# Kernel tuning notes

Measured on AMD Instinct MI355X. Metric: run time of the kernel, lower is better.

## Reference

```python
import jax, jax.numpy as jnp
import numpy as np

N = 50000      # nodes (single node type 'tx')
E = 400000     # edges per edge type ('fwd' and 'rev')
F_IN = 128     # input feature dim
F = 128        # cfg.gnn.dim_inner
H = 8          # attention heads
D = F // H     # per-head dim
L = 2          # cfg.gnn.layers_mp
C = 2          # dim_out (fraud logits)


def setup_inputs() -> dict:
    key = jax.random.key(0)
    k = jax.random.split(key, 12)
    f32 = jnp.float32
    g = lambda kk, sh, fan: jax.random.normal(kk, sh, f32) / np.float32(np.sqrt(fan))
    return dict(
        x=jax.random.normal(k[0], (N, F_IN), f32),
        edge_index_fwd=jax.random.randint(k[1], (2, E), 0, N),
        edge_index_rev=jax.random.randint(k[2], (2, E), 0, N),
        in_w=g(k[3], (F_IN, F), F_IN),
        in_b=jnp.zeros((F,), f32),
        kqv_w=g(k[4], (L, F, 3 * F), F),
        kqv_b=jnp.zeros((L, 3 * F), f32),
        krel_w=g(k[5], (L, 2, H, D, D), D),
        vrel_w=g(k[6], (L, 2, H, D, D), D),
        p_rel=jnp.ones((L, 2, H), f32),
        out_w=g(k[7], (L, F, F), F),
        out_b=jnp.zeros((L, F), f32),
        skip=jnp.ones((L,), f32),
        head_w=g(k[8], (F, C), F),
        head_b=jnp.zeros((C,), f32),
    )


def reference(x, edge_index_fwd, edge_index_rev, in_w, in_b, kqv_w, kqv_b,
              krel_w, vrel_w, p_rel, out_w, out_b, skip, head_w, head_b):
    n = x.shape[0]
    ef, er = edge_index_fwd, edge_index_rev
    Ef, Er = ef.shape[1], er.shape[1]
    dst = jnp.concatenate([ef[1], er[1]])                 # [E_tot]
    scale = 1.0 / jnp.sqrt(jnp.asarray(D, x.dtype))

    h = x @ in_w + in_b                                   # in_proj['tx'], [N,F]
    for l in range(L):
        kqv = h @ kqv_w[l] + kqv_b[l]                     # [N,3F]
        k, q, v = jnp.split(kqv, 3, axis=1)
        k = k.reshape(n, H, D)
        q = q.reshape(n, H, D)
        v = v.reshape(n, H, D)
        # per-edge-type relation transforms (head-wise DxD, no bias)
        k_rel = jnp.einsum('nhd,ehdf->enhf', k, krel_w[l])  # [2,N,H,D]
        v_rel = jnp.einsum('nhd,ehdf->enhf', v, vrel_w[l])
        # gather src features per edge type, concatenate edge types
        k_j = jnp.concatenate([k_rel[0][ef[0]], k_rel[1][er[0]]], axis=0)  # [E_tot,H,D]
        v_j = jnp.concatenate([v_rel[0][ef[0]], v_rel[1][er[0]]], axis=0)
        p_e = jnp.concatenate([jnp.broadcast_to(p_rel[l, 0], (Ef, H)),
                               jnp.broadcast_to(p_rel[l, 1], (Er, H))], axis=0)
        q_i = q[dst]                                       # [E_tot,H,D]
        alpha = jnp.einsum('ehd,ehd->eh', q_i, k_j) * p_e * scale
        # segment softmax over all incoming edges of each dst node
        m = jax.ops.segment_max(alpha, dst, num_segments=n)
        ex = jnp.exp(alpha - m[dst])
        denom = jax.ops.segment_sum(ex, dst, num_segments=n)
        w = ex / (denom[dst] + 1e-16)                      # [E_tot,H]
        agg = jax.ops.segment_sum(w[:, :, None] * v_j, dst,
                                  num_segments=n).reshape(n, F)
        a = jax.nn.gelu(agg, approximate=False) @ out_w[l] + out_b[l]
        g = jax.nn.sigmoid(skip[l])
        h = jax.nn.relu(g * a + (1.0 - g) * h)             # skip + act(dropout=0)
    return h @ head_w + head_b                             # logits [N,C]
```

## Files before the change

### kernel.cpp

```cpp
#include <hip/hip_runtime.h>
#include <math.h>

typedef short short8 __attribute__((ext_vector_type(8)));
typedef float f32x4 __attribute__((ext_vector_type(4)));

#define CAP 64

__device__ __forceinline__ unsigned short f2bf(float f){
    unsigned u = __float_as_uint(f);
    unsigned r = u + 0x7fffu + ((u >> 16) & 1u);
    return (unsigned short)(r >> 16);
}
__device__ __forceinline__ float bf2f(unsigned short s){
    return __uint_as_float((unsigned)s << 16);
}

__global__ void k_setup(const float* __restrict__ kqv_w, const float* __restrict__ kqv_b,
                        const float* __restrict__ krel_w, const float* __restrict__ vrel_w,
                        const float* __restrict__ p_rel, const float* __restrict__ out_w,
                        const float* __restrict__ out_b, const float* __restrict__ in_w,
                        const float* __restrict__ x, const float* __restrict__ head_b,
                        const int* __restrict__ ef, const int* __restrict__ er,
                        unsigned short* __restrict__ WcT, float* __restrict__ biasc,
                        unsigned short* __restrict__ WoT, float* __restrict__ biaso,
                        unsigned short* __restrict__ WiT, unsigned short* __restrict__ x16,
                        int* __restrict__ cnt, unsigned* __restrict__ srcs_pad,
                        float* __restrict__ logits, int n_nodes, int Ef, int Er)
{
    const long long E0 = Ef + Er;
    const long long N0 = E0 + 2*129*640;
    const long long N1 = N0 + 2*129*128;
    const long long N2 = N1 + 128*128;
    const long long N3 = N2 + (long long)n_nodes*32;
    const long long N4 = N3 + 2*n_nodes;

    for (long long idx = (long long)blockIdx.x*blockDim.x + threadIdx.x; idx < N4;
         idx += (long long)gridDim.x*blockDim.x) {
        if (idx < E0) {
            int e = (int)idx;
            int src, dst, tt;
            if (e < Ef) { src = ef[e]; dst = ef[Ef + e]; tt = 0; }
            else { int e2 = e - Ef; src = er[e2]; dst = er[Er + e2]; tt = 1; }
            int pos = atomicAdd(&cnt[dst], 1);
            if (pos < CAP)
                srcs_pad[dst*CAP + pos] = (unsigned)(tt*n_nodes + src)*32u;
        } else if (idx < N0) {
            int i = (int)(idx - E0);
            int l = i / (129*640);
            int rem = i % (129*640);
            int r = rem / 640, c = rem % 640;
            float val;
            if (c < 128) {
                val = (r < 128) ? kqv_w[((size_t)l*128 + r)*384 + 128 + c]
                                : kqv_b[l*384 + 128 + c];
            } else {
                int c2 = c - 128;
                int tt = c2 >> 8;
                int cc = c2 & 255;
                int f = cc >> 1;
                int part = cc & 1;
                int hh = f >> 4, fd = f & 15;
                const float* rw = (part == 0 ? krel_w : vrel_w)
                                  + (((size_t)(l*2 + tt)*8 + hh)*16)*16 + fd;
                int base_col = (part == 0 ? 0 : 256) + hh*16;
                float s = 0.f;
                #pragma unroll
                for (int d = 0; d < 16; ++d) {
                    float a = (r < 128) ? kqv_w[((size_t)l*128 + r)*384 + base_col + d]
                                        : kqv_b[l*384 + base_col + d];
                    s += a * rw[d*16];
                }
                if (part == 0) s *= p_rel[(l*2 + tt)*8 + hh] * 0.25f * 1.4426950408889634f;
                val = s;
            }
            if (r < 128) WcT[((size_t)l*640 + c)*128 + r] = f2bf(val);
            else         biasc[l*640 + c] = val;
        } else if (idx < N1) {
            int i = (int)(idx - N0);
            int l = i / (129*128);
            int rem = i % (129*128);
            int r = rem / 128, c = rem % 128;
            if (r < 128) WoT[((size_t)l*128 + c)*128 + r] = f2bf(out_w[((size_t)l*128 + r)*128 + c]);
            else         biaso[l*128 + c] = out_b[l*128 + c];
        } else if (idx < N2) {
            int i = (int)(idx - N1);
            int r = i >> 7, c = i & 127;
            WiT[(size_t)c*128 + r] = f2bf(in_w[(size_t)r*128 + c]);
        } else if (idx < N3) {
            long long i = idx - N2;
            float4 v = *(const float4*)&x[i*4];
            uint2 w;
            w.x = (unsigned)f2bf(v.x) | ((unsigned)f2bf(v.y) << 16);
            w.y = (unsigned)f2bf(v.z) | ((unsigned)f2bf(v.w) << 16);
            *(uint2*)&x16[i*4] = w;
        } else {
            long long i = idx - N3;
            logits[i] = head_b[i & 1];
        }
    }
}

__global__ __launch_bounds__(256) void k_mfma(
    const unsigned short* __restrict__ A16, const unsigned short* __restrict__ WT,
    const float* __restrict__ biasc, unsigned short* __restrict__ q16,
    unsigned short* __restrict__ h16, unsigned* __restrict__ kv,
    const float* __restrict__ skip, const float* __restrict__ hw,
    float* __restrict__ logits, int l,
    int n_nodes, int R, int C, int mode)
{
    __shared__ uint4 As[64*16];
    __shared__ uint4 Ws[64*16];
    int b = blockIdx.x;
    int xcd = b & 7, jj = b >> 3;
    int r_t = (jj / C)*8 + xcd;
    int c_t = jj % C;
    if (r_t >= R) return;
    int n0 = r_t*64, c0 = c_t*64;
    int t = threadIdx.x;

    #pragma unroll
    for (int it = 0; it < 4; ++it) {
        int gi = t + it*256;
        int m = gi >> 4, g = gi & 15;
        uint4 a = *(const uint4*)&A16[((size_t)(n0 + m)*16 + g)*8];
        As[m*16 + (g ^ (m & 15))] = a;
    }
    #pragma unroll
    for (int it = 0; it < 4; ++it) {
        int gi = t + it*256;
        int cw = gi >> 4, g = gi & 15;
        uint4 wv = *(const uint4*)&WT[((size_t)(c0 + cw)*16 + g)*8];
        Ws[cw*16 + (g ^ (cw & 15))] = wv;
    }
    __syncthreads();

    int lane = t & 63, w = t >> 6;
    int lm = lane & 15, quad = lane >> 4;
    f32x4 acc[4];
    #pragma unroll
    for (int i = 0; i < 4; ++i) { acc[i][0]=0.f; acc[i][1]=0.f; acc[i][2]=0.f; acc[i][3]=0.f; }

    #pragma unroll
    for (int chunk = 0; chunk < 4; ++chunk) {
        int gq = chunk*4 + quad;
        short8 bfrag = *(const short8*)&Ws[(w*16 + lm)*16 + (gq ^ lm)];
        #pragma unroll
        for (int i = 0; i < 4; ++i) {
            short8 afrag = *(const short8*)&As[(i*16 + lm)*16 + (gq ^ lm)];
            acc[i] = __builtin_amdgcn_mfma_f32_16x16x32_bf16(afrag, bfrag, acc[i], 0, 0, 0);
        }
    }

    int c = c0 + w*16 + lm;
    float bc = biasc[c];
    bool even = (lane & 1) == 0;
    if (mode == 3) {
        float g = 1.f/(1.f + expf(-skip[l]));
        float hw0 = hw[c*2], hw1 = hw[c*2 + 1];
        #pragma unroll
        for (int i = 0; i < 4; ++i) {
            #pragma unroll
            for (int rr = 0; rr < 4; ++rr) {
                int m = n0 + i*16 + quad*4 + rr;
                float nv = 0.f;
                if (m < n_nodes) {
                    float hv = bf2f(h16[(size_t)m*128 + c]);
                    nv = fmaxf(g*(acc[i][rr] + bc) + (1.f - g)*hv, 0.f);
                }
                float p0 = nv*hw0, p1 = nv*hw1;
                p0 += __shfl_xor(p0, 1); p1 += __shfl_xor(p1, 1);
                p0 += __shfl_xor(p0, 2); p1 += __shfl_xor(p1, 2);
                p0 += __shfl_xor(p0, 4); p1 += __shfl_xor(p1, 4);
                p0 += __shfl_xor(p0, 8); p1 += __shfl_xor(p1, 8);
                if (lm == 0 && m < n_nodes) {
                    atomicAdd(&logits[m*2],     p0);
                    atomicAdd(&logits[m*2 + 1], p1);
                }
            }
        }
    } else if (mode == 2) {
        float g = 1.f/(1.f + expf(-skip[l]));
        unsigned* dst = (unsigned*)h16;
        #pragma unroll
        for (int i = 0; i < 4; ++i) {
            #pragma unroll
            for (int rr = 0; rr < 4; ++rr) {
                int m = n0 + i*16 + quad*4 + rr;
                float hv = (m < n_nodes) ? bf2f(h16[(size_t)m*128 + c]) : 0.f;
                float nv = fmaxf(g*(acc[i][rr] + bc) + (1.f - g)*hv, 0.f);
                float other = __shfl_xor(nv, 1);
                if (even && m < n_nodes)
                    dst[(size_t)m*64 + (c >> 1)] =
                        (unsigned)f2bf(nv) | ((unsigned)f2bf(other) << 16);
            }
        }
    } else if (mode == 0) {
        unsigned* dst = (unsigned*)h16;
        #pragma unroll
        for (int i = 0; i < 4; ++i) {
            #pragma unroll
            for (int rr = 0; rr < 4; ++rr) {
                int m = n0 + i*16 + quad*4 + rr;
                float nv = acc[i][rr] + bc;
                float other = __shfl_xor(nv, 1);
                if (even && m < n_nodes)
                    dst[(size_t)m*64 + (c >> 1)] =
                        (unsigned)f2bf(nv) | ((unsigned)f2bf(other) << 16);
            }
        }
    } else if (c0 < 128) {
        unsigned* dst = (unsigned*)q16;
        #pragma unroll
        for (int i = 0; i < 4; ++i) {
            #pragma unroll
            for (int rr = 0; rr < 4; ++rr) {
                float val = acc[i][rr] + bc;
                float other = __shfl_xor(val, 1);
                int m = n0 + i*16 + quad*4 + rr;
                if (even && m < n_nodes)
                    dst[(size_t)m*64 + (c >> 1)] =
                        (unsigned)f2bf(val) | ((unsigned)f2bf(other) << 16);
            }
        }
    } else {
        int c2 = c - 128;
        int tt = c2 >> 8;
        int f = (c2 & 255) >> 1;
        unsigned* dst = kv + (size_t)tt*n_nodes*128;
        #pragma unroll
        for (int i = 0; i < 4; ++i) {
            #pragma unroll
            for (int rr = 0; rr < 4; ++rr) {
                float val = acc[i][rr] + bc;
                float other = __shfl_xor(val, 1);
                int m = n0 + i*16 + quad*4 + rr;
                if (even && m < n_nodes) {
                    unsigned wd = ((unsigned)f2bf(val) << 16) | (unsigned)f2bf(other);
                    dst[(size_t)m*128 + f] = wd;
                }
            }
        }
    }
}

__global__ __launch_bounds__(256) void k_attn(
    const unsigned* __restrict__ srcs_pad, const int* __restrict__ cnt,
    const uint4* __restrict__ kv, const unsigned short* __restrict__ q16,
    unsigned short* __restrict__ qa16, int n_base, int n_hi)
{
    int lane = threadIdx.x & 31;
    int n = n_base + blockIdx.x*8 + (threadIdx.x >> 5);
    if (n >= n_hi) return;
    uint2 qp = *(const uint2*)&q16[(size_t)n*128 + lane*4];
    float4 q4;
    q4.x = __uint_as_float(qp.x << 16);
    q4.y = __uint_as_float(qp.x & 0xffff0000u);
    q4.z = __uint_as_float(qp.y << 16);
    q4.w = __uint_as_float(qp.y & 0xffff0000u);
    int s = n*CAP, e = s + min(cnt[n], CAP);

    const uint4* kvl = kv + lane;
    const unsigned* srcs = srcs_pad;

    float lsum = 0.f;
    float4 a = make_float4(0.f, 0.f, 0.f, 0.f);

    unsigned sv0 = srcs[s],     sv1 = srcs[s + 1];
    unsigned sv2 = srcs[s + 2], sv3 = srcs[s + 3];
    uint4 w0 = kvl[sv0], w1 = kvl[sv1], w2 = kvl[sv2], w3 = kvl[sv3];

    int pos = s;

#define ATT_PAIR(wA, wB)                                                       \
    {                                                                          \
        float d0 = __uint_as_float(wA.x & 0xffff0000u)*q4.x                    \
                 + __uint_as_float(wA.y & 0xffff0000u)*q4.y                    \
                 + __uint_as_float(wA.z & 0xffff0000u)*q4.z                    \
                 + __uint_as_float(wA.w & 0xffff0000u)*q4.w;                   \
        float d1 = __uint_as_float(wB.x & 0xffff0000u)*q4.x                    \
                 + __uint_as_float(wB.y & 0xffff0000u)*q4.y                    \
                 + __uint_as_float(wB.z & 0xffff0000u)*q4.z                    \
                 + __uint_as_float(wB.w & 0xffff0000u)*q4.w;                   \
        d0 += __shfl_xor(d0, 1); d1 += __shfl_xor(d1, 1);                      \
        d0 += __shfl_xor(d0, 2); d1 += __shfl_xor(d1, 2);                      \
        float wt0 = exp2f(d0), wt1 = exp2f(d1);                                \
        lsum += wt0 + wt1;                                                     \
        a.x += wt0*__uint_as_float(wA.x << 16);                                \
        a.y += wt0*__uint_as_float(wA.y << 16);                                \
        a.z += wt0*__uint_as_float(wA.z << 16);                                \
        a.w += wt0*__uint_as_float(wA.w << 16);                                \
        a.x += wt1*__uint_as_float(wB.x << 16);                                \
        a.y += wt1*__uint_as_float(wB.y << 16);                                \
        a.z += wt1*__uint_as_float(wB.z << 16);                                \
        a.w += wt1*__uint_as_float(wB.w << 16);                                \
    }

#define ATT_ONE(wA)                                                            \
    {                                                                          \
        float d = __uint_as_float(wA.x & 0xffff0000u)*q4.x                     \
                + __uint_as_float(wA.y & 0xffff0000u)*q4.y                     \
                + __uint_as_float(wA.z & 0xffff0000u)*q4.z                     \
                + __uint_as_float(wA.w & 0xffff0000u)*q4.w;                    \
        d += __shfl_xor(d, 1);                                                 \
        d += __shfl_xor(d, 2);                                                 \
        float wt = exp2f(d);                                                   \
        lsum += wt;                                                            \
        a.x += wt*__uint_as_float(wA.x << 16);                                 \
        a.y += wt*__uint_as_float(wA.y << 16);                                 \
        a.z += wt*__uint_as_float(wA.z << 16);                                 \
        a.w += wt*__uint_as_float(wA.w << 16);                                 \
    }

    for (; pos + 3 < e; pos += 4) {
        unsigned p0 = srcs[pos + 4], p1 = srcs[pos + 5];
        ATT_PAIR(w0, w1);
        w0 = kvl[p0]; w1 = kvl[p1];
        unsigned p2 = srcs[pos + 6], p3 = srcs[pos + 7];
        ATT_PAIR(w2, w3);
        w2 = kvl[p2]; w3 = kvl[p3];
    }
    int rem = e - pos;
    if (rem > 0) {
        ATT_ONE(w0);
        if (rem > 1) ATT_ONE(w1);
        if (rem > 2) ATT_ONE(w2);
    }
#undef ATT_PAIR
#undef ATT_ONE

    float inv = 1.f/(lsum + 1e-16f);
    float x0 = a.x*inv, x1 = a.y*inv, x2 = a.z*inv, x3 = a.w*inv;
    float g0 = 0.5f*x0*(1.f + erff(x0*0.70710678118654752f));
    float g1 = 0.5f*x1*(1.f + erff(x1*0.70710678118654752f));
    float g2 = 0.5f*x2*(1.f + erff(x2*0.70710678118654752f));
    float g3 = 0.5f*x3*(1.f + erff(x3*0.70710678118654752f));
    uint2 pk;
    pk.x = (unsigned)f2bf(g0) | ((unsigned)f2bf(g1) << 16);
    pk.y = (unsigned)f2bf(g2) | ((unsigned)f2bf(g3) << 16);
    *(uint2*)&qa16[(size_t)n*128 + lane*4] = pk;
}

extern "C" void kernel_launch(void* const* d_in, const int* in_sizes, int n_in,
                              void* d_out, int out_size, void* d_ws, size_t ws_size,
                              hipStream_t stream)
{
    const float* x      = (const float*)d_in[0];
    const int*   ef     = (const int*)d_in[1];
    const int*   er     = (const int*)d_in[2];
    const float* in_w   = (const float*)d_in[3];
    const float* in_b   = (const float*)d_in[4];
    const float* kqv_w  = (const float*)d_in[5];
    const float* kqv_b  = (const float*)d_in[6];
    const float* krel_w = (const float*)d_in[7];
    const float* vrel_w = (const float*)d_in[8];
    const float* p_rel  = (const float*)d_in[9];
    const float* out_w  = (const float*)d_in[10];
    const float* out_b  = (const float*)d_in[11];
    const float* skip   = (const float*)d_in[12];
    const float* head_w = (const float*)d_in[13];
    const float* head_b = (const float*)d_in[14];
    float* out = (float*)d_out;

    int n_nodes = in_sizes[0] / 128;
    int Ef = in_sizes[1] / 2, Er = in_sizes[2] / 2;
    int ntile = (n_nodes + 63)/64;
    int npad = ntile*64;

    float* p = (float*)d_ws;
    unsigned* kv = (unsigned*)p; p += (size_t)2*n_nodes*128;
    unsigned short* h16  = (unsigned short*)p; p += (size_t)npad*128/2;
    unsigned short* q16  = (unsigned short*)p; p += (size_t)npad*128/2;
    unsigned short* qa16 = (unsigned short*)p; p += (size_t)npad*128/2;
    unsigned short* x16  = (unsigned short*)p; p += (size_t)npad*128/2;
    unsigned short* WiT = (unsigned short*)p; p += (size_t)(128*128)/2;
    unsigned short* WcT = (unsigned short*)p; p += (size_t)(2*640*128)/2;
    float* biasc = p; p += 2*640;
    unsigned short* WoT = (unsigned short*)p; p += (size_t)(2*128*128)/2;
    float* biaso = p; p += 2*128;
    int* cnt = (int*)p;            p += n_nodes;
    unsigned* srcs_pad = (unsigned*)p; p += (size_t)n_nodes*CAP;

    int Rg = (ntile + 7)/8;

    hipMemsetAsync(cnt, 0, (size_t)n_nodes*sizeof(int), stream);
    hipMemsetAsync(srcs_pad, 0, (size_t)n_nodes*CAP*sizeof(unsigned), stream);
    k_setup<<<7500, 256, 0, stream>>>(kqv_w, kqv_b, krel_w, vrel_w, p_rel, out_w, out_b,
                                      in_w, x, head_b, ef, er, WcT, biasc, WoT, biaso,
                                      WiT, x16, cnt, srcs_pad, out, n_nodes, Ef, Er);

    int nh = (((n_nodes + 1)/2) + 7) & ~7;
    if (nh > n_nodes) nh = n_nodes;

    k_mfma<<<Rg*8*2, 256, 0, stream>>>(x16, WiT, in_b, nullptr, h16, kv, skip,
                                       head_w, out, 0, n_nodes, ntile, 2, 0);
    for (int l = 0; l < 2; ++l) {
        k_mfma<<<Rg*8*10, 256, 0, stream>>>(h16, WcT + (size_t)l*640*128,
                                            biasc + l*640, q16, nullptr, kv, skip,
                                            head_w, out, l, n_nodes, ntile, 10, 1);
        k_attn<<<nh/8, 256, 0, stream>>>(srcs_pad, cnt, (const uint4*)kv, q16, qa16,
                                         0, nh);
        k_attn<<<(n_nodes - nh + 7)/8, 256, 0, stream>>>(srcs_pad, cnt, (const uint4*)kv,
                                                         q16, qa16, nh, n_nodes);
        int omode = (l == 1) ? 3 : 2;
        k_mfma<<<Rg*8*2, 256, 0, stream>>>(qa16, WoT + (size_t)l*128*128,
                                           biaso + l*128, nullptr, h16, kv, skip,
                                           head_w, out, l, n_nodes, ntile, 2, omode);
    }
}
```

Baseline: 394.6 us.

## Build padded adjacency via two-pass per-XCD binning with LDS scatter

Replaces the per-edge global atomic scatter into the padded source list with two passes. First, edges are appended to per-XCD, per-64-node-bin buffers. Then a new kernel gathers each bin, scatters entries into LDS slots using shared atomics, and writes srcs_pad and cnt coalesced. This also removes the large memset of srcs_pad and the cnt memset. The cost is an extra kernel launch and intermediate buffer traffic, and edges beyond a bin capacity of 512 per XCD are silently dropped.

Result: slower. 405.2 us (+2.7%).

```diff
diff --git a/kernel.cpp b/kernel.cpp
--- a/kernel.cpp
+++ b/kernel.cpp
@@ -5,6 +5,7 @@
 typedef float f32x4 __attribute__((ext_vector_type(4)));
 
 #define CAP 64
+#define BCAP 512
 
 __device__ __forceinline__ unsigned short f2bf(float f){
     unsigned u = __float_as_uint(f);
@@ -24,9 +25,13 @@
                         unsigned short* __restrict__ WcT, float* __restrict__ biasc,
                         unsigned short* __restrict__ WoT, float* __restrict__ biaso,
                         unsigned short* __restrict__ WiT, unsigned short* __restrict__ x16,
-                        int* __restrict__ cnt, unsigned* __restrict__ srcs_pad,
-                        float* __restrict__ logits, int n_nodes, int Ef, int Er)
+                        int* __restrict__ bcur, unsigned* __restrict__ bbuf,
+                        float* __restrict__ logits, int n_nodes, int Ef, int Er, int NB)
 {
+    int xcd;
+    asm volatile("s_getreg_b32 %0, hwreg(HW_REG_XCC_ID)" : "=s"(xcd));
+    xcd &= 7;
+
     const long long E0 = Ef + Er;
     const long long N0 = E0 + 2*129*640;
     const long long N1 = N0 + 2*129*128;
@@ -41,9 +46,12 @@
             int src, dst, tt;
             if (e < Ef) { src = ef[e]; dst = ef[Ef + e]; tt = 0; }
             else { int e2 = e - Ef; src = er[e2]; dst = er[Er + e2]; tt = 1; }
-            int pos = atomicAdd(&cnt[dst], 1);
-            if (pos < CAP)
-                srcs_pad[dst*CAP + pos] = (unsigned)(tt*n_nodes + src)*32u;
+            int r = dst >> 6;
+            int seg = xcd*NB + r;
+            int pos = atomicAdd(&bcur[seg], 1);
+            if (pos < BCAP)
+                bbuf[(size_t)seg*BCAP + pos] =
+                    (unsigned)(dst & 63) | ((unsigned)tt << 6) | ((unsigned)src << 7);
         } else if (idx < N0) {
             int i = (int)(idx - E0);
             int l = i / (129*640);
@@ -100,6 +108,44 @@
     }
 }
 
+__global__ __launch_bounds__(256) void k_bin2(
+    const unsigned* __restrict__ bbuf, const int* __restrict__ bcur,
+    unsigned* __restrict__ srcs_pad, int* __restrict__ cnt,
+    int n_nodes, int NB)
+{
+    __shared__ unsigned lslot[64*CAP];
+    __shared__ int lcnt[64];
+    int r = blockIdx.x;
+    int lo = r*64;
+    int m = min(64, n_nodes - lo);
+    if (m <= 0) return;
+    int t = threadIdx.x;
+    if (t < 64) lcnt[t] = 0;
+    __syncthreads();
+    for (int xc = 0; xc < 8; ++xc) {
+        int seg = xc*NB + r;
+        int n = min(bcur[seg], BCAP);
+        const unsigned* sp = &bbuf[(size_t)seg*BCAP];
+        for (int i = t; i < n; i += 256) {
+            unsigned w = sp[i];
+            int d = w & 63;
+            int p = atomicAdd(&lcnt[d], 1);
+            if (p < CAP) {
+                unsigned tt = (w >> 6) & 1u;
+                unsigned src = w >> 7;
+                lslot[d*CAP + p] = (tt*(unsigned)n_nodes + src)*32u;
+            }
+        }
+    }
+    __syncthreads();
+    for (int i = t; i < m*CAP; i += 256) {
+        int d = i >> 6, s = i & (CAP - 1);
+        int c = min(lcnt[d], CAP);
+        srcs_pad[(size_t)(lo + d)*CAP + s] = (s < c) ? lslot[d*CAP + s] : 0u;
+    }
+    if (t < m) cnt[lo + t] = min(lcnt[t], CAP);
+}
+
 __global__ __launch_bounds__(256) void k_mfma(
     const unsigned short* __restrict__ A16, const unsigned short* __restrict__ WT,
     const float* __restrict__ biasc, unsigned short* __restrict__ q16,
@@ -365,6 +411,7 @@
     int Ef = in_sizes[1] / 2, Er = in_sizes[2] / 2;
     int ntile = (n_nodes + 63)/64;
     int npad = ntile*64;
+    int NB = (n_nodes + 63)/64;
 
     float* p = (float*)d_ws;
     unsigned* kv = (unsigned*)p; p += (size_t)2*n_nodes*128;
@@ -378,15 +425,17 @@
     unsigned short* WoT = (unsigned short*)p; p += (size_t)(2*128*128)/2;
     float* biaso = p; p += 2*128;
     int* cnt = (int*)p;            p += n_nodes;
+    int* bcur = (int*)p;           p += (size_t)8*NB;
+    unsigned* bbuf = (unsigned*)p; p += (size_t)8*NB*BCAP;
     unsigned* srcs_pad = (unsigned*)p; p += (size_t)n_nodes*CAP;
 
     int Rg = (ntile + 7)/8;
 
-    hipMemsetAsync(cnt, 0, (size_t)n_nodes*sizeof(int), stream);
-    hipMemsetAsync(srcs_pad, 0, (size_t)n_nodes*CAP*sizeof(unsigned), stream);
+    hipMemsetAsync(bcur, 0, (size_t)8*NB*sizeof(int), stream);
     k_setup<<<7500, 256, 0, stream>>>(kqv_w, kqv_b, krel_w, vrel_w, p_rel, out_w, out_b,
                                       in_w, x, head_b, ef, er, WcT, biasc, WoT, biaso,
-                                      WiT, x16, cnt, srcs_pad, out, n_nodes, Ef, Er);
+                                      WiT, x16, bcur, bbuf, out, n_nodes, Ef, Er, NB);
+    k_bin2<<<NB, 256, 0, stream>>>(bbuf, bcur, srcs_pad, cnt, n_nodes, NB);
 
     int nh = (((n_nodes + 1)/2) + 7) & ~7;
     if (nh > n_nodes) nh = n_nodes;
```

## Fuse input projection GEMM into setup kernel, converting x and in_w on the fly

Applied to the files above, without the earlier changes.

The separate input-projection MFMA launch and the x/in_w bf16 conversion passes are removed. The setup work and the input GEMM now run in one kernel: the first NITB blocks do edge bucketing, weight preprocessing and logits init, and the remaining blocks load fp32 x and in_w directly, convert them to bf16 into shared memory and run the MFMA. This saves one launch and the round trip of writing and rereading the x16 copy. The GEMM blocks now read fp32 inputs and do strided in_w loads, and the two kinds of blocks share one grid.

Result: slower. 416.2 us (+5.5%).

```diff
diff --git a/kernel.cpp b/kernel.cpp
--- a/kernel.cpp
+++ b/kernel.cpp
@@ -5,6 +5,7 @@
 typedef float f32x4 __attribute__((ext_vector_type(4)));
 
 #define CAP 64
+#define NITB 2048
 
 __device__ __forceinline__ unsigned short f2bf(float f){
     unsigned u = __float_as_uint(f);
@@ -15,87 +16,153 @@
     return __uint_as_float((unsigned)s << 16);
 }
 
-__global__ void k_setup(const float* __restrict__ kqv_w, const float* __restrict__ kqv_b,
-                        const float* __restrict__ krel_w, const float* __restrict__ vrel_w,
-                        const float* __restrict__ p_rel, const float* __restrict__ out_w,
-                        const float* __restrict__ out_b, const float* __restrict__ in_w,
-                        const float* __restrict__ x, const float* __restrict__ head_b,
-                        const int* __restrict__ ef, const int* __restrict__ er,
-                        unsigned short* __restrict__ WcT, float* __restrict__ biasc,
-                        unsigned short* __restrict__ WoT, float* __restrict__ biaso,
-                        unsigned short* __restrict__ WiT, unsigned short* __restrict__ x16,
-                        int* __restrict__ cnt, unsigned* __restrict__ srcs_pad,
-                        float* __restrict__ logits, int n_nodes, int Ef, int Er)
+__global__ __launch_bounds__(256) void k_front(
+        const float* __restrict__ kqv_w, const float* __restrict__ kqv_b,
+        const float* __restrict__ krel_w, const float* __restrict__ vrel_w,
+        const float* __restrict__ p_rel, const float* __restrict__ out_w,
+        const float* __restrict__ out_b, const float* __restrict__ in_w,
+        const float* __restrict__ in_b, const float* __restrict__ x,
+        const float* __restrict__ head_b,
+        const int* __restrict__ ef, const int* __restrict__ er,
+        unsigned short* __restrict__ WcT, float* __restrict__ biasc,
+        unsigned short* __restrict__ WoT, float* __restrict__ biaso,
+        int* __restrict__ cnt, unsigned* __restrict__ srcs_pad,
+        unsigned short* __restrict__ h16, float* __restrict__ logits,
+        int n_nodes, int Ef, int Er, int R)
 {
-    const long long E0 = Ef + Er;
-    const long long N0 = E0 + 2*129*640;
-    const long long N1 = N0 + 2*129*128;
-    const long long N2 = N1 + 128*128;
-    const long long N3 = N2 + (long long)n_nodes*32;
-    const long long N4 = N3 + 2*n_nodes;
-
-    for (long long idx = (long long)blockIdx.x*blockDim.x + threadIdx.x; idx < N4;
-         idx += (long long)gridDim.x*blockDim.x) {
-        if (idx < E0) {
-            int e = (int)idx;
-            int src, dst, tt;
-            if (e < Ef) { src = ef[e]; dst = ef[Ef + e]; tt = 0; }
-            else { int e2 = e - Ef; src = er[e2]; dst = er[Er + e2]; tt = 1; }
-            int pos = atomicAdd(&cnt[dst], 1);
-            if (pos < CAP)
-                srcs_pad[dst*CAP + pos] = (unsigned)(tt*n_nodes + src)*32u;
-        } else if (idx < N0) {
-            int i = (int)(idx - E0);
-            int l = i / (129*640);
-            int rem = i % (129*640);
-            int r = rem / 640, c = rem % 640;
-            float val;
-            if (c < 128) {
-                val = (r < 128) ? kqv_w[((size_t)l*128 + r)*384 + 128 + c]
-                                : kqv_b[l*384 + 128 + c];
+    if (blockIdx.x < NITB) {
+        const long long E0 = Ef + Er;
+        const long long M0 = E0 + 2*129*640;
+        const long long M1 = M0 + 2*129*128;
+        const long long M2 = M1 + 2*n_nodes;
+
+        for (long long idx = (long long)blockIdx.x*256 + threadIdx.x; idx < M2;
+             idx += (long long)NITB*256) {
+            if (idx < E0) {
+                int e = (int)idx;
+                int src, dst, tt;
+                if (e < Ef) { src = ef[e]; dst = ef[Ef + e]; tt = 0; }
+                else { int e2 = e - Ef; src = er[e2]; dst = er[Er + e2]; tt = 1; }
+                int pos = atomicAdd(&cnt[dst], 1);
+                if (pos < CAP)
+                    srcs_pad[dst*CAP + pos] = (unsigned)(tt*n_nodes + src)*32u;
+            } else if (idx < M0) {
+                int i = (int)(idx - E0);
+                int l = i / (129*640);
+                int rem = i % (129*640);
+                int r = rem / 640, c = rem % 640;
+                float val;
+                if (c < 128) {
+                    val = (r < 128) ? kqv_w[((size_t)l*128 + r)*384 + 128 + c]
+                                    : kqv_b[l*384 + 128 + c];
+                } else {
+                    int c2 = c - 128;
+                    int tt = c2 >> 8;
+                    int cc = c2 & 255;
+                    int f = cc >> 1;
+                    int part = cc & 1;
+                    int hh = f >> 4, fd = f & 15;
+                    const float* rw = (part == 0 ? krel_w : vrel_w)
+                                      + (((size_t)(l*2 + tt)*8 + hh)*16)*16 + fd;
+                    int base_col = (part == 0 ? 0 : 256) + hh*16;
+                    float s = 0.f;
+                    #pragma unroll
+                    for (int d = 0; d < 16; ++d) {
+                        float a = (r < 128) ? kqv_w[((size_t)l*128 + r)*384 + base_col + d]
+                                            : kqv_b[l*384 + base_col + d];
+                        s += a * rw[d*16];
+                    }
+                    if (part == 0) s *= p_rel[(l*2 + tt)*8 + hh] * 0.25f * 1.4426950408889634f;
+                    val = s;
+                }
+                if (r < 128) WcT[((size_t)l*640 + c)*128 + r] = f2bf(val);
+                else         biasc[l*640 + c] = val;
+            } else if (idx < M1) {
+                int i = (int)(idx - M0);
+                int l = i / (129*128);
+                int rem = i % (129*128);
+                int r = rem / 128, c = rem % 128;
+                if (r < 128) WoT[((size_t)l*128 + c)*128 + r] = f2bf(out_w[((size_t)l*128 + r)*128 + c]);
+                else         biaso[l*128 + c] = out_b[l*128 + c];
             } else {
-                int c2 = c - 128;
-                int tt = c2 >> 8;
-                int cc = c2 & 255;
-                int f = cc >> 1;
-                int part = cc & 1;
-                int hh = f >> 4, fd = f & 15;
-                const float* rw = (part == 0 ? krel_w : vrel_w)
-                                  + (((size_t)(l*2 + tt)*8 + hh)*16)*16 + fd;
-                int base_col = (part == 0 ? 0 : 256) + hh*16;
-                float s = 0.f;
-                #pragma unroll
-                for (int d = 0; d < 16; ++d) {
-                    float a = (r < 128) ? kqv_w[((size_t)l*128 + r)*384 + base_col + d]
-                                        : kqv_b[l*384 + base_col + d];
-                    s += a * rw[d*16];
-                }
-                if (part == 0) s *= p_rel[(l*2 + tt)*8 + hh] * 0.25f * 1.4426950408889634f;
-                val = s;
+                long long i = idx - M1;
+                logits[i] = head_b[i & 1];
             }
-            if (r < 128) WcT[((size_t)l*640 + c)*128 + r] = f2bf(val);
-            else         biasc[l*640 + c] = val;
-        } else if (idx < N1) {
-            int i = (int)(idx - N0);
-            int l = i / (129*128);
-            int rem = i % (129*128);
-            int r = rem / 128, c = rem % 128;
-            if (r < 128) WoT[((size_t)l*128 + c)*128 + r] = f2bf(out_w[((size_t)l*128 + r)*128 + c]);
-            else         biaso[l*128 + c] = out_b[l*128 + c];
-        } else if (idx < N2) {
-            int i = (int)(idx - N1);
-            int r = i >> 7, c = i & 127;
-            WiT[(size_t)c*128 + r] = f2bf(in_w[(size_t)r*128 + c]);
-        } else if (idx < N3) {
-            long long i = idx - N2;
-            float4 v = *(const float4*)&x[i*4];
-            uint2 w;
-            w.x = (unsigned)f2bf(v.x) | ((unsigned)f2bf(v.y) << 16);
-            w.y = (unsigned)f2bf(v.z) | ((unsigned)f2bf(v.w) << 16);
-            *(uint2*)&x16[i*4] = w;
-        } else {
-            long long i = idx - N3;
-            logits[i] = head_b[i & 1];
+        }
+        return;
+    }
+
+    __shared__ uint4 As[64*16];
+    __shared__ uint4 Ws[64*16];
+    int b = blockIdx.x - NITB;
+    int xcd = b & 7, jj = b >> 3;
+    int r_t = (jj / 2)*8 + xcd;
+    int c_t = jj % 2;
+    if (r_t >= R) return;
+    int n0 = r_t*64, c0 = c_t*64;
+    int t = threadIdx.x;
+
+    #pragma unroll
+    for (int it = 0; it < 4; ++it) {
+        int gi = t + it*256;
+        int m = gi >> 4, g = gi & 15;
+        int row = min(n0 + m, n_nodes - 1);
+        const float* xp = &x[(size_t)row*128 + g*8];
+        float4 v0 = *(const float4*)xp;
+        float4 v1 = *(const float4*)(xp + 4);
+        uint4 a;
+        a.x = (unsigned)f2bf(v0.x) | ((unsigned)f2bf(v0.y) << 16);
+        a.y = (unsigned)f2bf(v0.z) | ((unsigned)f2bf(v0.w) << 16);
+        a.z = (unsigned)f2bf(v1.x) | ((unsigned)f2bf(v1.y) << 16);
+        a.w = (unsigned)f2bf(v1.z) | ((unsigned)f2bf(v1.w) << 16);
+        As[m*16 + (g ^ (m & 15))] = a;
+    }
+    #pragma unroll
+    for (int it = 0; it < 4; ++it) {
+        int gi = t + it*256;
+        int cw = gi >> 4, g = gi & 15;
+        int col = c0 + cw;
+        const float* wp = &in_w[(size_t)(g*8)*128 + col];
+        uint4 wv;
+        wv.x = (unsigned)f2bf(wp[0])     | ((unsigned)f2bf(wp[128])   << 16);
+        wv.y = (unsigned)f2bf(wp[2*128]) | ((unsigned)f2bf(wp[3*128]) << 16);
+        wv.z = (unsigned)f2bf(wp[4*128]) | ((unsigned)f2bf(wp[5*128]) << 16);
+        wv.w = (unsigned)f2bf(wp[6*128]) | ((unsigned)f2bf(wp[7*128]) << 16);
+        Ws[cw*16 + (g ^ (cw & 15))] = wv;
+    }
+    __syncthreads();
+
+    int lane = t & 63, w = t >> 6;
+    int lm = lane & 15, quad = lane >> 4;
+    f32x4 acc[4];
+    #pragma unroll
+    for (int i = 0; i < 4; ++i) { acc[i][0]=0.f; acc[i][1]=0.f; acc[i][2]=0.f; acc[i][3]=0.f; }
+
+    #pragma unroll
+    for (int chunk = 0; chunk < 4; ++chunk) {
+        int gq = chunk*4 + quad;
+        short8 bfrag = *(const short8*)&Ws[(w*16 + lm)*16 + (gq ^ lm)];
+        #pragma unroll
+        for (int i = 0; i < 4; ++i) {
+            short8 afrag = *(const short8*)&As[(i*16 + lm)*16 + (gq ^ lm)];
+            acc[i] = __builtin_amdgcn_mfma_f32_16x16x32_bf16(afrag, bfrag, acc[i], 0, 0, 0);
+        }
+    }
+
+    int c = c0 + w*16 + lm;
+    float bc = in_b[c];
+    bool even = (lane & 1) == 0;
+    unsigned* dst = (unsigned*)h16;
+    #pragma unroll
+    for (int i = 0; i < 4; ++i) {
+        #pragma unroll
+        for (int rr = 0; rr < 4; ++rr) {
+            int m = n0 + i*16 + quad*4 + rr;
+            float nv = acc[i][rr] + bc;
+            float other = __shfl_xor(nv, 1);
+            if (even && m < n_nodes)
+                dst[(size_t)m*64 + (c >> 1)] =
+                    (unsigned)f2bf(nv) | ((unsigned)f2bf(other) << 16);
         }
     }
 }
@@ -188,20 +255,6 @@
                 int m = n0 + i*16 + quad*4 + rr;
                 float hv = (m < n_nodes) ? bf2f(h16[(size_t)m*128 + c]) : 0.f;
                 float nv = fmaxf(g*(acc[i][rr] + bc) + (1.f - g)*hv, 0.f);
-                float other = __shfl_xor(nv, 1);
-                if (even && m < n_nodes)
-                    dst[(size_t)m*64 + (c >> 1)] =
-                        (unsigned)f2bf(nv) | ((unsigned)f2bf(other) << 16);
-            }
-        }
-    } else if (mode == 0) {
-        unsigned* dst = (unsigned*)h16;
-        #pragma unroll
-        for (int i = 0; i < 4; ++i) {
-            #pragma unroll
-            for (int rr = 0; rr < 4; ++rr) {
-                int m = n0 + i*16 + quad*4 + rr;
-                float nv = acc[i][rr] + bc;
                 float other = __shfl_xor(nv, 1);
                 if (even && m < n_nodes)
                     dst[(size_t)m*64 + (c >> 1)] =
@@ -371,8 +424,6 @@
     unsigned short* h16  = (unsigned short*)p; p += (size_t)npad*128/2;
     unsigned short* q16  = (unsigned short*)p; p += (size_t)npad*128/2;
     unsigned short* qa16 = (unsigned short*)p; p += (size_t)npad*128/2;
-    unsigned short* x16  = (unsigned short*)p; p += (size_t)npad*128/2;
-    unsigned short* WiT = (unsigned short*)p; p += (size_t)(128*128)/2;
     unsigned short* WcT = (unsigned short*)p; p += (size_t)(2*640*128)/2;
     float* biasc = p; p += 2*640;
     unsigned short* WoT = (unsigned short*)p; p += (size_t)(2*128*128)/2;
@@ -384,15 +435,15 @@
 
     hipMemsetAsync(cnt, 0, (size_t)n_nodes*sizeof(int), stream);
     hipMemsetAsync(srcs_pad, 0, (size_t)n_nodes*CAP*sizeof(unsigned), stream);
-    k_setup<<<7500, 256, 0, stream>>>(kqv_w, kqv_b, krel_w, vrel_w, p_rel, out_w, out_b,
-                                      in_w, x, head_b, ef, er, WcT, biasc, WoT, biaso,
-                                      WiT, x16, cnt, srcs_pad, out, n_nodes, Ef, Er);
+    k_front<<<NITB + Rg*8*2, 256, 0, stream>>>(kqv_w, kqv_b, krel_w, vrel_w, p_rel,
+                                               out_w, out_b, in_w, in_b, x, head_b,
+                                               ef, er, WcT, biasc, WoT, biaso,
+                                               cnt, srcs_pad, h16, out,
+                                               n_nodes, Ef, Er, ntile);
 
     int nh = (((n_nodes + 1)/2) + 7) & ~7;
     if (nh > n_nodes) nh = n_nodes;
 
-    k_mfma<<<Rg*8*2, 256, 0, stream>>>(x16, WiT, in_b, nullptr, h16, kv, skip,
-                                       head_w, out, 0, n_nodes, ntile, 2, 0);
     for (int l = 0; l < 2; ++l) {
         k_mfma<<<Rg*8*10, 256, 0, stream>>>(h16, WcT + (size_t)l*640*128,
                                             biasc + l*640, q16, nullptr, kv, skip,
```
